# Kernel optimization log

Measured on AMD Instinct MI355X. Metric: run time of the kernel, lower is better.

The kernel has to match this reference:

```python
import jax, jax.numpy as jnp
import numpy as np


def setup_inputs() -> dict:
    key = jax.random.key(0)
    ks = jax.random.split(key, 6)
    B, S, D, U = 32, 2048, 1024, 1024
    scale = 1.0 / np.sqrt(D)
    return {
        "h_enc": jax.random.normal(ks[0], (B, S, D), dtype=jnp.float32),
        "h_dec": jax.random.normal(ks[1], (B, D), dtype=jnp.float32),
        "W_enc": jax.random.normal(ks[2], (D, U), dtype=jnp.float32) * scale,
        "b_enc": jnp.zeros((U,), dtype=jnp.float32),
        "W_dec": jax.random.normal(ks[3], (D, U), dtype=jnp.float32) * scale,
        "b_dec": jnp.zeros((U,), dtype=jnp.float32),
        "W_com": jax.random.normal(ks[4], (U, 1), dtype=jnp.float32) * (1.0 / np.sqrt(U)),
        "b_com": jnp.zeros((1,), dtype=jnp.float32),
    }


def reference(h_enc, h_dec, W_enc, b_enc, W_dec, b_dec, W_com, b_com):
    # h_enc: [B,S,D] -> projected enc features [B,S,U]
    enc_p = jnp.einsum("bsd,du->bsu", h_enc, W_enc) + b_enc
    # h_dec: [B,D] -> [B,1,U]
    dec_p = (h_dec @ W_dec + b_dec)[:, None, :]
    # additive score: [B,S,1]
    score = jnp.einsum("bsu,uo->bso", jnp.tanh(dec_p + enc_p), W_com) + b_com
    attn = jax.nn.softmax(score, axis=1)  # softmax over seq axis
    # NOTE: original code multiplies attn by the PROJECTED h_enc (reassigned)
    context_vec = jnp.sum(attn * enc_p, axis=1)  # [B,U]
    return (context_vec, attn)
```

## Files before the change

kernel.cpp:

```cpp
#include <hip/hip_runtime.h>
#include <math.h>
#include <stdint.h>

#define Bz 32
#define Sz 2048
#define Dz 1024
#define Uz 1024
#define Mz (Bz*Sz)

typedef __attribute__((ext_vector_type(8))) short bf16x8;
typedef __attribute__((ext_vector_type(4))) float f32x4;

__device__ __forceinline__ unsigned short f2bf(float f) {
    union { float f; uint32_t u; } v; v.f = f;
    uint32_t r = v.u + 0x7FFFu + ((v.u >> 16) & 1u);
    return (unsigned short)(r >> 16);
}

__device__ __forceinline__ float fast_tanh(float x) {
    float e = __expf(2.f * x);
    return 1.f - 2.f * __builtin_amdgcn_rcpf(e + 1.f);
}

#define GLD16(gsrc, ldst) \
    __builtin_amdgcn_global_load_lds((__attribute__((address_space(1))) void*)(void*)(gsrc), \
        (__attribute__((address_space(3))) void*)(ldst), 16, 0, 0)

#define CONV_BLOCKS 16384
#define WT_BLOCKS   256
#define DECI_BLOCKS 32
#define SINIT_BLOCKS 64

__global__ __launch_bounds__(256) void prep_kernel(
    const float* __restrict__ h_enc, unsigned short* __restrict__ hbf,
    const float* __restrict__ W_enc, unsigned short* __restrict__ wT,
    const float* __restrict__ b_dec, float* __restrict__ dec_p,
    const float* __restrict__ b_com, float* __restrict__ score)
{
    __shared__ float tile[64][65];
    const int bid = blockIdx.x;
    const int tid = threadIdx.x;
    if (bid < CONV_BLOCKS) {
        const size_t i = ((size_t)bid * 256 + tid) * 16;
#pragma unroll
        for (int h = 0; h < 2; ++h) {
            const float4 a = *(const float4*)(h_enc + i + h * 8);
            const float4 c = *(const float4*)(h_enc + i + h * 8 + 4);
            union { unsigned short s[8]; uint4 v; } o;
            o.s[0] = f2bf(a.x); o.s[1] = f2bf(a.y); o.s[2] = f2bf(a.z); o.s[3] = f2bf(a.w);
            o.s[4] = f2bf(c.x); o.s[5] = f2bf(c.y); o.s[6] = f2bf(c.z); o.s[7] = f2bf(c.w);
            *(uint4*)(hbf + i + h * 8) = o.v;
        }
    } else if (bid < CONV_BLOCKS + WT_BLOCKS) {
        const int b2 = bid - CONV_BLOCKS;
        const int c  = tid & 63;
        const int r0 = tid >> 6;
        const int u0 = (b2 & 15) * 64;
        const int d0 = (b2 >> 4) * 64;
        for (int r = r0; r < 64; r += 4)
            tile[r][c] = W_enc[(size_t)(d0 + r) * Uz + u0 + c];
        __syncthreads();
        for (int r = r0; r < 64; r += 4)
            wT[(size_t)(u0 + r) * Dz + d0 + c] = f2bf(tile[c][r]);
    } else if (bid < CONV_BLOCKS + WT_BLOCKS + DECI_BLOCKS) {
        const int b3 = bid - (CONV_BLOCKS + WT_BLOCKS);
        const int u4 = tid * 4;
        *(float4*)&dec_p[b3 * Uz + u4] = *(const float4*)&b_dec[u4];
    } else {
        const int b4 = bid - (CONV_BLOCKS + WT_BLOCKS + DECI_BLOCKS);
        const float bc = b_com[0];
        const int i4 = (b4 * 256 + tid) * 4;
        float4 v = {bc, bc, bc, bc};
        *(float4*)&score[i4] = v;
    }
}

__global__ __launch_bounds__(256) void dec_partial_kernel(
    const float* __restrict__ h_dec, const float* __restrict__ W_dec,
    float* __restrict__ dec_p)
{
    __shared__ float hs[128];
    const int b  = blockIdx.x >> 3;
    const int d0 = (blockIdx.x & 7) * 128;
    const int tid = threadIdx.x;
    const int u4 = tid * 4;
    if (tid < 128) hs[tid] = h_dec[b * Dz + d0 + tid];
    __syncthreads();
    float4 acc = {0.f, 0.f, 0.f, 0.f};
#pragma unroll 4
    for (int d = 0; d < 128; ++d) {
        const float  a = hs[d];
        const float4 w = *(const float4*)&W_dec[(size_t)(d0 + d) * Uz + u4];
        acc.x += a * w.x; acc.y += a * w.y; acc.z += a * w.z; acc.w += a * w.w;
    }
    float* o = dec_p + b * Uz + u4;
    atomicAdd(o + 0, acc.x); atomicAdd(o + 1, acc.y);
    atomicAdd(o + 2, acc.z); atomicAdd(o + 3, acc.w);
}

__global__ __launch_bounds__(256) void score_mfma_kernel(
    const unsigned short* __restrict__ hbf,
    const unsigned short* __restrict__ wT,
    const float* __restrict__ dec_p,
    const float* __restrict__ W_com,
    float* __restrict__ score)
{
    __shared__ unsigned short As[8 * 512];
    __shared__ unsigned short Bs[8 * 512];

    const int tid  = threadIdx.x;
    const int w    = tid >> 6;
    const int lane = tid & 63;
    const int ln   = lane & 15;
    const int q    = lane >> 4;
    const int wm   = w & 1;
    const int wn   = w >> 1;

    const int xcd = blockIdx.x & 7;
    const int idx = blockIdx.x >> 3;
    const int mb  = xcd * 64 + (idx >> 3);
    const int m0  = mb * 128;
    const int ub  = (idx & 7) * 128;
    const int b   = m0 / Sz;

    const int g0 = 2 * w;
    const unsigned short* a_src0 = hbf + (size_t)(m0 + g0 * 16 + ln) * Dz + q * 8;
    const unsigned short* a_src1 = a_src0 + (size_t)16 * Dz;
    const unsigned short* b_src0 = wT + (size_t)(ub + g0 * 16 + ln) * Dz + q * 8;
    const unsigned short* b_src1 = b_src0 + (size_t)16 * Dz;
    unsigned short* a_dst0 = As + g0 * 512;
    unsigned short* a_dst1 = a_dst0 + 512;
    unsigned short* b_dst0 = Bs + g0 * 512;
    unsigned short* b_dst1 = b_dst0 + 512;

    f32x4 acc[4][4];
#pragma unroll
    for (int i = 0; i < 4; ++i)
#pragma unroll
        for (int j = 0; j < 4; ++j) acc[i][j] = (f32x4){0.f, 0.f, 0.f, 0.f};

    for (int k0 = 0; k0 < Dz; k0 += 32) {
        __syncthreads();
        GLD16(a_src0 + k0, a_dst0);
        GLD16(a_src1 + k0, a_dst1);
        GLD16(b_src0 + k0, b_dst0);
        GLD16(b_src1 + k0, b_dst1);
        __syncthreads();

        bf16x8 af[4], bfr[4];
#pragma unroll
        for (int i = 0; i < 4; ++i)
            af[i] = *(const bf16x8*)(As + (wm * 4 + i) * 512 + lane * 8);
#pragma unroll
        for (int j = 0; j < 4; ++j)
            bfr[j] = *(const bf16x8*)(Bs + (wn * 4 + j) * 512 + lane * 8);
#pragma unroll
        for (int i = 0; i < 4; ++i)
#pragma unroll
            for (int j = 0; j < 4; ++j)
                acc[i][j] = __builtin_amdgcn_mfma_f32_16x16x32_bf16(
                    af[i], bfr[j], acc[i][j], 0, 0, 0);
    }

    float dpv[4], wcv[4];
#pragma unroll
    for (int j = 0; j < 4; ++j) {
        const int u = ub + (wn * 4 + j) * 16 + ln;
        dpv[j] = dec_p[b * Uz + u];
        wcv[j] = W_com[u];
    }
    float racc[4][4];
#pragma unroll
    for (int i = 0; i < 4; ++i)
#pragma unroll
        for (int r = 0; r < 4; ++r) {
            float v = 0.f;
#pragma unroll
            for (int j = 0; j < 4; ++j)
                v += fast_tanh(acc[i][j][r] + dpv[j]) * wcv[j];
            racc[i][r] = v;
        }

#pragma unroll
    for (int off = 1; off < 16; off <<= 1)
#pragma unroll
        for (int i = 0; i < 4; ++i)
#pragma unroll
            for (int r = 0; r < 4; ++r)
                racc[i][r] += __shfl_xor(racc[i][r], off, 64);
    if (ln == 0) {
#pragma unroll
        for (int i = 0; i < 4; ++i)
#pragma unroll
            for (int r = 0; r < 4; ++r)
                atomicAdd(&score[m0 + wm * 64 + i * 16 + q * 4 + r], racc[i][r]);
    }
}

__global__ __launch_bounds__(256) void softmax_init_kernel(
    const float* __restrict__ score, float* __restrict__ attn,
    const float* __restrict__ b_enc, float* __restrict__ out_ctx,
    float* __restrict__ wsum)
{
    __shared__ float red[256];
    const int tid = threadIdx.x;
    if (blockIdx.x >= 2 * Bz) {
        const int b3 = blockIdx.x - 2 * Bz;
        float4 z = {0.f, 0.f, 0.f, 0.f};
        *(float4*)&wsum[b3 * Dz + tid * 4] = z;
        return;
    }
    if (blockIdx.x >= Bz) {
        const int b2 = blockIdx.x - Bz;
        const int u4 = tid * 4;
        *(float4*)&out_ctx[b2 * Uz + u4] = *(const float4*)&b_enc[u4];
        return;
    }
    const int b = blockIdx.x;
    const float* srow = score + b * Sz;
    float v[8];
    float lm = -1e30f;
#pragma unroll
    for (int i = 0; i < 8; ++i) { v[i] = srow[i * 256 + tid]; lm = fmaxf(lm, v[i]); }
    red[tid] = lm; __syncthreads();
    for (int off = 128; off > 0; off >>= 1) {
        if (tid < off) red[tid] = fmaxf(red[tid], red[tid + off]);
        __syncthreads();
    }
    const float mx = red[0];
    __syncthreads();
    float ls = 0.f;
#pragma unroll
    for (int i = 0; i < 8; ++i) { v[i] = expf(v[i] - mx); ls += v[i]; }
    red[tid] = ls; __syncthreads();
    for (int off = 128; off > 0; off >>= 1) {
        if (tid < off) red[tid] += red[tid + off];
        __syncthreads();
    }
    const float inv = 1.f / red[0];
#pragma unroll
    for (int i = 0; i < 8; ++i) attn[b * Sz + i * 256 + tid] = v[i] * inv;
}

__global__ __launch_bounds__(256) void wsum_kernel(
    const float* __restrict__ h_enc, const float* __restrict__ attn,
    float* __restrict__ wsum)
{
    __shared__ float aw[64];
    const int b  = blockIdx.x >> 5;
    const int s0 = (blockIdx.x & 31) * 64;
    const int tid = threadIdx.x;
    if (tid < 64) aw[tid] = attn[b * Sz + s0 + tid];
    __syncthreads();
    float4 acc = {0.f, 0.f, 0.f, 0.f};
    const float* base = h_enc + ((size_t)b * Sz + s0) * Dz + tid * 4;
#pragma unroll 4
    for (int s = 0; s < 64; ++s) {
        const float a = aw[s];
        const float4 h = *(const float4*)(base + (size_t)s * Dz);
        acc.x += a * h.x; acc.y += a * h.y; acc.z += a * h.z; acc.w += a * h.w;
    }
    float* o = wsum + b * Dz + tid * 4;
    atomicAdd(o + 0, acc.x); atomicAdd(o + 1, acc.y);
    atomicAdd(o + 2, acc.z); atomicAdd(o + 3, acc.w);
}

__global__ __launch_bounds__(256) void ctx_partial_kernel(
    const float* __restrict__ wsum, const float* __restrict__ W_enc,
    float* __restrict__ out_ctx)
{
    __shared__ float hs[128];
    const int b  = blockIdx.x >> 3;
    const int d0 = (blockIdx.x & 7) * 128;
    const int tid = threadIdx.x;
    const int u4 = tid * 4;
    if (tid < 128) hs[tid] = wsum[b * Dz + d0 + tid];
    __syncthreads();
    float4 acc = {0.f, 0.f, 0.f, 0.f};
#pragma unroll 4
    for (int d = 0; d < 128; ++d) {
        const float  a = hs[d];
        const float4 wv = *(const float4*)&W_enc[(size_t)(d0 + d) * Uz + u4];
        acc.x += a * wv.x; acc.y += a * wv.y; acc.z += a * wv.z; acc.w += a * wv.w;
    }
    float* o = out_ctx + b * Uz + u4;
    atomicAdd(o + 0, acc.x); atomicAdd(o + 1, acc.y);
    atomicAdd(o + 2, acc.z); atomicAdd(o + 3, acc.w);
}

__global__ __launch_bounds__(256) void dec_proj_kernel(
    const float* __restrict__ h_dec, const float* __restrict__ W_dec,
    const float* __restrict__ b_dec, float* __restrict__ dec_p)
{
    __shared__ float hs[Dz];
    const int b = blockIdx.x >> 2;
    const int u = ((blockIdx.x & 3) << 8) + threadIdx.x;
    for (int d = threadIdx.x; d < Dz; d += 256) hs[d] = h_dec[b * Dz + d];
    __syncthreads();
    float acc = 0.f;
#pragma unroll 4
    for (int d = 0; d < Dz; ++d) acc += hs[d] * W_dec[d * Uz + u];
    dec_p[b * Uz + u] = acc + b_dec[u];
}

#define MT 64
#define NT 64
#define KT 64
__global__ __launch_bounds__(256) void score_kernel(
    const float* __restrict__ h_enc, const float* __restrict__ W_enc,
    const float* __restrict__ dec_p, const float* __restrict__ W_com,
    const float* __restrict__ b_com, float* __restrict__ score)
{
    __shared__ __align__(16) float As[KT][MT + 4];
    __shared__ __align__(16) float Bs[KT][NT + 4];
    __shared__ float red[MT][17];
    const int tid = threadIdx.x;
    const int tx = tid & 15;
    const int ty = tid >> 4;
    const int m0 = blockIdx.x * MT;
    const int b  = m0 / Sz;
    float s_acc = 0.f;
    for (int u0 = 0; u0 < Uz; u0 += NT) {
        float acc[4][4];
#pragma unroll
        for (int i = 0; i < 4; ++i)
#pragma unroll
            for (int j = 0; j < 4; ++j) acc[i][j] = 0.f;
        for (int k0 = 0; k0 < Dz; k0 += KT) {
            __syncthreads();
#pragma unroll
            for (int i = 0; i < 4; ++i) {
                const int row = ty + i * 16;
                const int c4  = tx * 4;
                const float4 v = *(const float4*)&h_enc[(size_t)(m0 + row) * Dz + k0 + c4];
                As[c4 + 0][row] = v.x; As[c4 + 1][row] = v.y;
                As[c4 + 2][row] = v.z; As[c4 + 3][row] = v.w;
            }
#pragma unroll
            for (int i = 0; i < 4; ++i) {
                const int row = ty + i * 16;
                *(float4*)&Bs[row][tx * 4] =
                    *(const float4*)&W_enc[(size_t)(k0 + row) * Uz + u0 + tx * 4];
            }
            __syncthreads();
#pragma unroll 8
            for (int k = 0; k < KT; ++k) {
                const float4 a = *(const float4*)&As[k][ty * 4];
                const float4 wv = *(const float4*)&Bs[k][tx * 4];
                acc[0][0] += a.x * wv.x; acc[0][1] += a.x * wv.y; acc[0][2] += a.x * wv.z; acc[0][3] += a.x * wv.w;
                acc[1][0] += a.y * wv.x; acc[1][1] += a.y * wv.y; acc[1][2] += a.y * wv.z; acc[1][3] += a.y * wv.w;
                acc[2][0] += a.z * wv.x; acc[2][1] += a.z * wv.y; acc[2][2] += a.z * wv.z; acc[2][3] += a.z * wv.w;
                acc[3][0] += a.w * wv.x; acc[3][1] += a.w * wv.y; acc[3][2] += a.w * wv.z; acc[3][3] += a.w * wv.w;
            }
        }
        const float4 dp = *(const float4*)&dec_p[b * Uz + u0 + tx * 4];
        const float4 wc = *(const float4*)&W_com[u0 + tx * 4];
#pragma unroll
        for (int i = 0; i < 4; ++i) {
            const float p = tanhf(acc[i][0] + dp.x) * wc.x + tanhf(acc[i][1] + dp.y) * wc.y
                          + tanhf(acc[i][2] + dp.z) * wc.z + tanhf(acc[i][3] + dp.w) * wc.w;
            red[ty * 4 + i][tx] = p;
        }
        __syncthreads();
        if (tid < MT) {
            float t = 0.f;
#pragma unroll
            for (int j = 0; j < 16; ++j) t += red[tid][j];
            s_acc += t;
        }
    }
    if (tid < MT) score[m0 + tid] = s_acc + b_com[0];
}

__global__ __launch_bounds__(256) void ctx_kernel(
    const float* __restrict__ wsum, const float* __restrict__ W_enc,
    const float* __restrict__ b_enc, float* __restrict__ out)
{
    __shared__ float hs[Dz];
    const int b = blockIdx.x >> 2;
    const int u = ((blockIdx.x & 3) << 8) + threadIdx.x;
    for (int d = threadIdx.x; d < Dz; d += 256) hs[d] = wsum[b * Dz + d];
    __syncthreads();
    float acc = 0.f;
#pragma unroll 4
    for (int d = 0; d < Dz; ++d) acc += hs[d] * W_enc[d * Uz + u];
    out[b * Uz + u] = acc + b_enc[u];
}

extern "C" void kernel_launch(void* const* d_in, const int* in_sizes, int n_in,
                              void* d_out, int out_size, void* d_ws, size_t ws_size,
                              hipStream_t stream)
{
    const float* h_enc = (const float*)d_in[0];
    const float* h_dec = (const float*)d_in[1];
    const float* W_enc = (const float*)d_in[2];
    const float* b_enc = (const float*)d_in[3];
    const float* W_dec = (const float*)d_in[4];
    const float* b_dec = (const float*)d_in[5];
    const float* W_com = (const float*)d_in[6];
    const float* b_com = (const float*)d_in[7];

    float* out_ctx  = (float*)d_out;
    float* out_attn = out_ctx + Bz * Uz;

    const size_t HBF_BYTES = (size_t)Mz * Dz * 2;
    const size_t WT_BYTES  = (size_t)Uz * Dz * 2;
    const size_t SMALL     = (size_t)(Bz*Uz + Bz*Sz + Bz*Dz) * 4;
    const size_t need      = HBF_BYTES + WT_BYTES + SMALL;

    if (ws_size >= need) {
        char* wsb = (char*)d_ws;
        unsigned short* hbf = (unsigned short*)wsb;
        unsigned short* wT  = (unsigned short*)(wsb + HBF_BYTES);
        float* dec_p = (float*)(wsb + HBF_BYTES + WT_BYTES);
        float* score = dec_p + Bz * Uz;
        float* wsum  = score + Bz * Sz;

        prep_kernel<<<CONV_BLOCKS + WT_BLOCKS + DECI_BLOCKS + SINIT_BLOCKS, 256, 0, stream>>>(
            h_enc, hbf, W_enc, wT, b_dec, dec_p, b_com, score);
        dec_partial_kernel<<<Bz * 8, 256, 0, stream>>>(h_dec, W_dec, dec_p);
        score_mfma_kernel<<<(Mz / 128) * (Uz / 128), 256, 0, stream>>>(hbf, wT, dec_p, W_com, score);
        softmax_init_kernel<<<3 * Bz, 256, 0, stream>>>(score, out_attn, b_enc, out_ctx, wsum);
        wsum_kernel<<<Bz * 32, 256, 0, stream>>>(h_enc, out_attn, wsum);
        ctx_partial_kernel<<<Bz * 8, 256, 0, stream>>>(wsum, W_enc, out_ctx);
    } else {
        float* ws    = (float*)d_ws;
        float* dec_p = ws;
        float* score = ws + Bz * Uz;
        float* wsum  = ws + Bz * Uz + Bz * Sz;

        dec_proj_kernel<<<(Bz * Uz) / 256, 256, 0, stream>>>(h_dec, W_dec, b_dec, dec_p);
        score_kernel<<<Mz / MT, 256, 0, stream>>>(h_enc, W_enc, dec_p, W_com, b_com, score);
        softmax_init_kernel<<<3 * Bz, 256, 0, stream>>>(score, out_attn, b_enc, out_ctx, wsum);
        wsum_kernel<<<Bz * 32, 256, 0, stream>>>(h_enc, out_attn, wsum);
        ctx_kernel<<<(Bz * Uz) / 256, 256, 0, stream>>>(wsum, W_enc, b_enc, out_ctx);
    }
}
```

Baseline: 778.6 us.

## Double K-step per barrier in score GEMM and drop atomics in wsum reduction

The MFMA score kernel now loads a 64-wide K slice per iteration, doubling the LDS tiles, which halves the number of barrier pairs per tile. The wsum kernel is restructured so each block owns 128 output columns for one batch and reduces the full sequence in two halves through shared memory. This removes the wsum zero-init blocks and the float atomics, at the cost of far fewer blocks (256) and scalar, non-vectorized loads of h_enc, which may lower achieved bandwidth.

```diff
diff --git a/kernel.cpp b/kernel.cpp
--- a/kernel.cpp
+++ b/kernel.cpp
@@ -105,8 +105,8 @@
     const float* __restrict__ W_com,
     float* __restrict__ score)
 {
-    __shared__ unsigned short As[8 * 512];
-    __shared__ unsigned short Bs[8 * 512];
+    __shared__ unsigned short As[16 * 512];
+    __shared__ unsigned short Bs[16 * 512];
 
     const int tid  = threadIdx.x;
     const int w    = tid >> 6;
@@ -123,15 +123,14 @@
     const int ub  = (idx & 7) * 128;
     const int b   = m0 / Sz;
 
-    const int g0 = 2 * w;
-    const unsigned short* a_src0 = hbf + (size_t)(m0 + g0 * 16 + ln) * Dz + q * 8;
+    const unsigned short* a_src0 = hbf + (size_t)(m0 + (2 * w) * 16 + ln) * Dz + q * 8;
     const unsigned short* a_src1 = a_src0 + (size_t)16 * Dz;
-    const unsigned short* b_src0 = wT + (size_t)(ub + g0 * 16 + ln) * Dz + q * 8;
+    const unsigned short* b_src0 = wT + (size_t)(ub + (2 * w) * 16 + ln) * Dz + q * 8;
     const unsigned short* b_src1 = b_src0 + (size_t)16 * Dz;
-    unsigned short* a_dst0 = As + g0 * 512;
-    unsigned short* a_dst1 = a_dst0 + 512;
-    unsigned short* b_dst0 = Bs + g0 * 512;
-    unsigned short* b_dst1 = b_dst0 + 512;
+    unsigned short* a_dst0 = As + (4 * w) * 512;
+    unsigned short* a_dst1 = As + (4 * w + 2) * 512;
+    unsigned short* b_dst0 = Bs + (4 * w) * 512;
+    unsigned short* b_dst1 = Bs + (4 * w + 2) * 512;
 
     f32x4 acc[4][4];
 #pragma unroll
@@ -139,27 +138,34 @@
 #pragma unroll
         for (int j = 0; j < 4; ++j) acc[i][j] = (f32x4){0.f, 0.f, 0.f, 0.f};
 
-    for (int k0 = 0; k0 < Dz; k0 += 32) {
-        __syncthreads();
-        GLD16(a_src0 + k0, a_dst0);
-        GLD16(a_src1 + k0, a_dst1);
-        GLD16(b_src0 + k0, b_dst0);
-        GLD16(b_src1 + k0, b_dst1);
-        __syncthreads();
-
-        bf16x8 af[4], bfr[4];
-#pragma unroll
-        for (int i = 0; i < 4; ++i)
-            af[i] = *(const bf16x8*)(As + (wm * 4 + i) * 512 + lane * 8);
-#pragma unroll
-        for (int j = 0; j < 4; ++j)
-            bfr[j] = *(const bf16x8*)(Bs + (wn * 4 + j) * 512 + lane * 8);
-#pragma unroll
-        for (int i = 0; i < 4; ++i)
+    for (int k0 = 0; k0 < Dz; k0 += 64) {
+        __syncthreads();
+        GLD16(a_src0 + k0,      a_dst0);
+        GLD16(a_src0 + k0 + 32, a_dst0 + 512);
+        GLD16(a_src1 + k0,      a_dst1);
+        GLD16(a_src1 + k0 + 32, a_dst1 + 512);
+        GLD16(b_src0 + k0,      b_dst0);
+        GLD16(b_src0 + k0 + 32, b_dst0 + 512);
+        GLD16(b_src1 + k0,      b_dst1);
+        GLD16(b_src1 + k0 + 32, b_dst1 + 512);
+        __syncthreads();
+
+#pragma unroll
+        for (int kh = 0; kh < 2; ++kh) {
+            bf16x8 af[4], bfr[4];
+#pragma unroll
+            for (int i = 0; i < 4; ++i)
+                af[i] = *(const bf16x8*)(As + ((wm * 4 + i) * 2 + kh) * 512 + lane * 8);
 #pragma unroll
             for (int j = 0; j < 4; ++j)
-                acc[i][j] = __builtin_amdgcn_mfma_f32_16x16x32_bf16(
-                    af[i], bfr[j], acc[i][j], 0, 0, 0);
+                bfr[j] = *(const bf16x8*)(Bs + ((wn * 4 + j) * 2 + kh) * 512 + lane * 8);
+#pragma unroll
+            for (int i = 0; i < 4; ++i)
+#pragma unroll
+                for (int j = 0; j < 4; ++j)
+                    acc[i][j] = __builtin_amdgcn_mfma_f32_16x16x32_bf16(
+                        af[i], bfr[j], acc[i][j], 0, 0, 0);
+        }
     }
 
     float dpv[4], wcv[4];
@@ -199,17 +205,10 @@
 
 __global__ __launch_bounds__(256) void softmax_init_kernel(
     const float* __restrict__ score, float* __restrict__ attn,
-    const float* __restrict__ b_enc, float* __restrict__ out_ctx,
-    float* __restrict__ wsum)
+    const float* __restrict__ b_enc, float* __restrict__ out_ctx)
 {
     __shared__ float red[256];
     const int tid = threadIdx.x;
-    if (blockIdx.x >= 2 * Bz) {
-        const int b3 = blockIdx.x - 2 * Bz;
-        float4 z = {0.f, 0.f, 0.f, 0.f};
-        *(float4*)&wsum[b3 * Dz + tid * 4] = z;
-        return;
-    }
     if (blockIdx.x >= Bz) {
         const int b2 = blockIdx.x - Bz;
         const int u4 = tid * 4;
@@ -246,23 +245,27 @@
     const float* __restrict__ h_enc, const float* __restrict__ attn,
     float* __restrict__ wsum)
 {
-    __shared__ float aw[64];
-    const int b  = blockIdx.x >> 5;
-    const int s0 = (blockIdx.x & 31) * 64;
-    const int tid = threadIdx.x;
-    if (tid < 64) aw[tid] = attn[b * Sz + s0 + tid];
-    __syncthreads();
-    float4 acc = {0.f, 0.f, 0.f, 0.f};
-    const float* base = h_enc + ((size_t)b * Sz + s0) * Dz + tid * 4;
+    __shared__ float aw[Sz];
+    __shared__ float red[256];
+    const int b    = blockIdx.x >> 3;
+    const int d0   = (blockIdx.x & 7) * 128;
+    const int tid  = threadIdx.x;
+    const int half = tid >> 7;
+    const int dl   = tid & 127;
+    const int d    = d0 + dl;
+
+    for (int i = tid; i < Sz; i += 256) aw[i] = attn[b * Sz + i];
+    __syncthreads();
+
+    const float* base = h_enc + ((size_t)b * Sz + half * 1024) * Dz + d;
+    float acc = 0.f;
 #pragma unroll 4
-    for (int s = 0; s < 64; ++s) {
-        const float a = aw[s];
-        const float4 h = *(const float4*)(base + (size_t)s * Dz);
-        acc.x += a * h.x; acc.y += a * h.y; acc.z += a * h.z; acc.w += a * h.w;
-    }
-    float* o = wsum + b * Dz + tid * 4;
-    atomicAdd(o + 0, acc.x); atomicAdd(o + 1, acc.y);
-    atomicAdd(o + 2, acc.z); atomicAdd(o + 3, acc.w);
+    for (int s = 0; s < 1024; ++s)
+        acc += aw[half * 1024 + s] * base[(size_t)s * Dz];
+    red[tid] = acc;
+    __syncthreads();
+    if (tid < 128)
+        wsum[b * Dz + d] = red[tid] + red[tid + 128];
 }
 
 __global__ __launch_bounds__(256) void ctx_partial_kernel(
@@ -420,8 +423,8 @@
             h_enc, hbf, W_enc, wT, b_dec, dec_p, b_com, score);
         dec_partial_kernel<<<Bz * 8, 256, 0, stream>>>(h_dec, W_dec, dec_p);
         score_mfma_kernel<<<(Mz / 128) * (Uz / 128), 256, 0, stream>>>(hbf, wT, dec_p, W_com, score);
-        softmax_init_kernel<<<3 * Bz, 256, 0, stream>>>(score, out_attn, b_enc, out_ctx, wsum);
-        wsum_kernel<<<Bz * 32, 256, 0, stream>>>(h_enc, out_attn, wsum);
+        softmax_init_kernel<<<2 * Bz, 256, 0, stream>>>(score, out_attn, b_enc, out_ctx);
+        wsum_kernel<<<Bz * 8, 256, 0, stream>>>(h_enc, out_attn, wsum);
         ctx_partial_kernel<<<Bz * 8, 256, 0, stream>>>(wsum, W_enc, out_ctx);
     } else {
         float* ws    = (float*)d_ws;
@@ -431,8 +434,8 @@
 
         dec_proj_kernel<<<(Bz * Uz) / 256, 256, 0, stream>>>(h_dec, W_dec, b_dec, dec_p);
         score_kernel<<<Mz / MT, 256, 0, stream>>>(h_enc, W_enc, dec_p, W_com, b_com, score);
-        softmax_init_kernel<<<3 * Bz, 256, 0, stream>>>(score, out_attn, b_enc, out_ctx, wsum);
-        wsum_kernel<<<Bz * 32, 256, 0, stream>>>(h_enc, out_attn, wsum);
+        softmax_init_kernel<<<2 * Bz, 256, 0, stream>>>(score, out_attn, b_enc, out_ctx);
+        wsum_kernel<<<Bz * 8, 256, 0, stream>>>(h_enc, out_attn, wsum);
         ctx_kernel<<<(Bz * Uz) / 256, 256, 0, stream>>>(wsum, W_enc, b_enc, out_ctx);
     }
 }
```

Measured after the change: 877.4 us. +12.7%, slower.

## Enlarge score GEMM tiles to 256x256 with double-buffered LDS and K=64 stages

Applied to the files above, without the earlier changes.

Reworks the bf16 MFMA score GEMM to use 512-thread blocks computing 256x256 tiles with 8x4 MFMA accumulators per wave, instead of 128x128 tiles. LDS is double-buffered with 64-wide K stages so the global-to-LDS loads for the next stage overlap the current MFMAs, and there is one barrier per stage. Per-block partial scores are reduced across waves in shared memory before a single atomicAdd per row, which cuts global atomics. In exchange, register and LDS use per block rise considerably (128 accumulator VGPRs, about 132KB of LDS), which may limit occupancy or cause spills.

```diff
diff --git a/kernel.cpp b/kernel.cpp
--- a/kernel.cpp
+++ b/kernel.cpp
@@ -98,80 +98,97 @@
     atomicAdd(o + 2, acc.z); atomicAdd(o + 3, acc.w);
 }
 
-__global__ __launch_bounds__(256) void score_mfma_kernel(
+__global__ __launch_bounds__(512, 2) void score_mfma_kernel(
     const unsigned short* __restrict__ hbf,
     const unsigned short* __restrict__ wT,
     const float* __restrict__ dec_p,
     const float* __restrict__ W_com,
     float* __restrict__ score)
 {
-    __shared__ unsigned short As[8 * 512];
-    __shared__ unsigned short Bs[8 * 512];
+    __shared__ unsigned short As[2][32 * 512];
+    __shared__ unsigned short Bs[2][32 * 512];
+    __shared__ float sred[4][256];
 
     const int tid  = threadIdx.x;
     const int w    = tid >> 6;
     const int lane = tid & 63;
     const int ln   = lane & 15;
     const int q    = lane >> 4;
-    const int wm   = w & 1;
-    const int wn   = w >> 1;
+    const int wm   = w >> 2;
+    const int wn   = w & 3;
 
     const int xcd = blockIdx.x & 7;
     const int idx = blockIdx.x >> 3;
-    const int mb  = xcd * 64 + (idx >> 3);
-    const int m0  = mb * 128;
-    const int ub  = (idx & 7) * 128;
+    const int mb  = xcd * 32 + (idx >> 2);
+    const int m0  = mb * 256;
+    const int ub  = (idx & 3) * 256;
     const int b   = m0 / Sz;
 
-    const int g0 = 2 * w;
-    const unsigned short* a_src0 = hbf + (size_t)(m0 + g0 * 16 + ln) * Dz + q * 8;
-    const unsigned short* a_src1 = a_src0 + (size_t)16 * Dz;
-    const unsigned short* b_src0 = wT + (size_t)(ub + g0 * 16 + ln) * Dz + q * 8;
-    const unsigned short* b_src1 = b_src0 + (size_t)16 * Dz;
-    unsigned short* a_dst0 = As + g0 * 512;
-    unsigned short* a_dst1 = a_dst0 + 512;
-    unsigned short* b_dst0 = Bs + g0 * 512;
-    unsigned short* b_dst1 = b_dst0 + 512;
-
-    f32x4 acc[4][4];
-#pragma unroll
-    for (int i = 0; i < 4; ++i)
+    const unsigned short* aA0 = hbf + (size_t)(m0 + w * 32 + ln) * Dz + q * 8;
+    const unsigned short* aA1 = aA0 + (size_t)16 * Dz;
+    const unsigned short* bB0 = wT + (size_t)(ub + w * 32 + ln) * Dz + q * 8;
+    const unsigned short* bB1 = bB0 + (size_t)16 * Dz;
+
+#define STAGE(nb_, k0_) do { \
+        unsigned short* ad = &As[nb_][(w * 4) * 512]; \
+        unsigned short* bd = &Bs[nb_][(w * 4) * 512]; \
+        GLD16(aA0 + (k0_),      ad); \
+        GLD16(aA0 + (k0_) + 32, ad + 512); \
+        GLD16(aA1 + (k0_),      ad + 1024); \
+        GLD16(aA1 + (k0_) + 32, ad + 1536); \
+        GLD16(bB0 + (k0_),      bd); \
+        GLD16(bB0 + (k0_) + 32, bd + 512); \
+        GLD16(bB1 + (k0_),      bd + 1024); \
+        GLD16(bB1 + (k0_) + 32, bd + 1536); \
+    } while (0)
+
+    f32x4 acc[8][4];
+#pragma unroll
+    for (int i = 0; i < 8; ++i)
 #pragma unroll
         for (int j = 0; j < 4; ++j) acc[i][j] = (f32x4){0.f, 0.f, 0.f, 0.f};
 
-    for (int k0 = 0; k0 < Dz; k0 += 32) {
+#define COMPUTE(cb_) do { \
+        _Pragma("unroll") \
+        for (int kh = 0; kh < 2; ++kh) { \
+            bf16x8 af[8], bfr[4]; \
+            _Pragma("unroll") \
+            for (int i = 0; i < 8; ++i) \
+                af[i] = *(const bf16x8*)(&As[cb_][(((wm * 8 + i) << 1) + kh) * 512 + lane * 8]); \
+            _Pragma("unroll") \
+            for (int j = 0; j < 4; ++j) \
+                bfr[j] = *(const bf16x8*)(&Bs[cb_][(((wn * 4 + j) << 1) + kh) * 512 + lane * 8]); \
+            _Pragma("unroll") \
+            for (int i = 0; i < 8; ++i) \
+                _Pragma("unroll") \
+                for (int j = 0; j < 4; ++j) \
+                    acc[i][j] = __builtin_amdgcn_mfma_f32_16x16x32_bf16( \
+                        af[i], bfr[j], acc[i][j], 0, 0, 0); \
+        } \
+    } while (0)
+
+    STAGE(0, 0);
+    __syncthreads();
+
+    int nb = 0;
+    for (int t = 0; t < 15; ++t) {
+        STAGE(nb ^ 1, (t + 1) * 64);
+        COMPUTE(nb);
         __syncthreads();
-        GLD16(a_src0 + k0, a_dst0);
-        GLD16(a_src1 + k0, a_dst1);
-        GLD16(b_src0 + k0, b_dst0);
-        GLD16(b_src1 + k0, b_dst1);
-        __syncthreads();
-
-        bf16x8 af[4], bfr[4];
-#pragma unroll
-        for (int i = 0; i < 4; ++i)
-            af[i] = *(const bf16x8*)(As + (wm * 4 + i) * 512 + lane * 8);
-#pragma unroll
-        for (int j = 0; j < 4; ++j)
-            bfr[j] = *(const bf16x8*)(Bs + (wn * 4 + j) * 512 + lane * 8);
-#pragma unroll
-        for (int i = 0; i < 4; ++i)
-#pragma unroll
-            for (int j = 0; j < 4; ++j)
-                acc[i][j] = __builtin_amdgcn_mfma_f32_16x16x32_bf16(
-                    af[i], bfr[j], acc[i][j], 0, 0, 0);
-    }
+        nb ^= 1;
+    }
+    COMPUTE(nb);
 
     float dpv[4], wcv[4];
 #pragma unroll
     for (int j = 0; j < 4; ++j) {
-        const int u = ub + (wn * 4 + j) * 16 + ln;
+        const int u = ub + wn * 64 + j * 16 + ln;
         dpv[j] = dec_p[b * Uz + u];
         wcv[j] = W_com[u];
     }
-    float racc[4][4];
-#pragma unroll
-    for (int i = 0; i < 4; ++i)
+    float racc[8][4];
+#pragma unroll
+    for (int i = 0; i < 8; ++i)
 #pragma unroll
         for (int r = 0; r < 4; ++r) {
             float v = 0.f;
@@ -180,21 +197,27 @@
                 v += fast_tanh(acc[i][j][r] + dpv[j]) * wcv[j];
             racc[i][r] = v;
         }
-
 #pragma unroll
     for (int off = 1; off < 16; off <<= 1)
 #pragma unroll
-        for (int i = 0; i < 4; ++i)
+        for (int i = 0; i < 8; ++i)
 #pragma unroll
             for (int r = 0; r < 4; ++r)
                 racc[i][r] += __shfl_xor(racc[i][r], off, 64);
     if (ln == 0) {
 #pragma unroll
-        for (int i = 0; i < 4; ++i)
+        for (int i = 0; i < 8; ++i)
 #pragma unroll
             for (int r = 0; r < 4; ++r)
-                atomicAdd(&score[m0 + wm * 64 + i * 16 + q * 4 + r], racc[i][r]);
-    }
+                sred[wn][wm * 128 + i * 16 + q * 4 + r] = racc[i][r];
+    }
+    __syncthreads();
+    if (tid < 256) {
+        const float s = sred[0][tid] + sred[1][tid] + sred[2][tid] + sred[3][tid];
+        atomicAdd(&score[m0 + tid], s);
+    }
+#undef STAGE
+#undef COMPUTE
 }
 
 __global__ __launch_bounds__(256) void softmax_init_kernel(
@@ -419,7 +442,7 @@
         prep_kernel<<<CONV_BLOCKS + WT_BLOCKS + DECI_BLOCKS + SINIT_BLOCKS, 256, 0, stream>>>(
             h_enc, hbf, W_enc, wT, b_dec, dec_p, b_com, score);
         dec_partial_kernel<<<Bz * 8, 256, 0, stream>>>(h_dec, W_dec, dec_p);
-        score_mfma_kernel<<<(Mz / 128) * (Uz / 128), 256, 0, stream>>>(hbf, wT, dec_p, W_com, score);
+        score_mfma_kernel<<<(Mz / 256) * (Uz / 256), 512, 0, stream>>>(hbf, wT, dec_p, W_com, score);
         softmax_init_kernel<<<3 * Bz, 256, 0, stream>>>(score, out_attn, b_enc, out_ctx, wsum);
         wsum_kernel<<<Bz * 32, 256, 0, stream>>>(h_enc, out_attn, wsum);
         ctx_partial_kernel<<<Bz * 8, 256, 0, stream>>>(wsum, W_enc, out_ctx);
```

After: 705.1 us. 9.4% less time.
